# Kernel tuning notes

Hardware: AMD Instinct MI355X
Metric: run time of the kernel (lower is better)

## Reference

```python
import jax, jax.numpy as jnp
import numpy as np

VOCAB, E, S, H, L = 32000, 1024, 2048, 16, 2
HS = E // H  # head_size = 64
EPS = 1e-5


def setup_inputs() -> dict:
    key = jax.random.key(0)
    ks = jax.random.split(key, 12)
    sc = 0.02
    inp = {
        "seq": jax.random.randint(ks[0], (S,), 0, VOCAB, dtype=jnp.int64)
        if jax.config.jax_enable_x64 else jax.random.randint(ks[0], (S,), 0, VOCAB, dtype=jnp.int32),
        "tok_emb": jax.random.normal(ks[1], (VOCAB, E), jnp.float32) * sc,
        "pos_emb": jax.random.normal(ks[2], (S, E), jnp.float32) * sc,
        "Wq": jax.random.normal(ks[3], (L, H, E, HS), jnp.float32) * sc,
        "Wk": jax.random.normal(ks[4], (L, H, E, HS), jnp.float32) * sc,
        "Wv": jax.random.normal(ks[5], (L, H, E, HS), jnp.float32) * sc,
        "Wr": jax.random.normal(ks[6], (L, E, E), jnp.float32) * sc,
        "br": jnp.zeros((L, E), jnp.float32),
        "W1": jax.random.normal(ks[7], (L, E, 4 * E), jnp.float32) * sc,
        "b1": jnp.zeros((L, 4 * E), jnp.float32),
        "W2": jax.random.normal(ks[8], (L, 4 * E, E), jnp.float32) * sc,
        "b2": jnp.zeros((L, E), jnp.float32),
        "ln_g": jnp.ones((L, E), jnp.float32),
        "ln_b": jnp.zeros((L, E), jnp.float32),
    }
    return inp


def _layer_norm(x, g, b):
    mu = jnp.mean(x, axis=-1, keepdims=True)
    var = jnp.mean(jnp.square(x - mu), axis=-1, keepdims=True)
    return (x - mu) * jax.lax.rsqrt(var + EPS) * g + b


def reference(seq, tok_emb, pos_emb, Wq, Wk, Wv, Wr, br, W1, b1, W2, b2, ln_g, ln_b):
    # embeddings: [S, E]
    x = tok_emb[seq] + pos_emb
    att_maps = []
    for l in range(L):
        # NOTE: the torch Block reuses the SAME LayerNorm instance twice per block.
        x = _layer_norm(x, ln_g[l], ln_b[l])
        # per-head projections: [H, S, HS]
        q = jnp.einsum('se,hed->hsd', x, Wq[l])
        k = jnp.einsum('se,hed->hsd', x, Wk[l])
        v = jnp.einsum('se,hed->hsd', x, Wv[l])
        # unmasked (encoder) attention, full [H, S, S] scores
        atts = jax.nn.softmax(jnp.einsum('hsd,htd->hst', q, k) / np.sqrt(HS), axis=-1)
        av = jnp.einsum('hst,htd->hsd', atts, v)  # [H, S, HS]
        cat = jnp.transpose(av, (1, 0, 2)).reshape(S, H * HS)  # concat heads -> [S, E]
        x = x + cat @ Wr[l] + br[l]
        x = _layer_norm(x, ln_g[l], ln_b[l])
        x = x + jax.nn.relu(x @ W1[l] + b1[l]) @ W2[l] + b2[l]
        att_maps.append(atts)
    return x, jnp.stack(att_maps)  # ([S,E], [L,H,S,S])
```

## Files before the change

kernel.cpp:

```cpp
#include <hip/hip_runtime.h>
#include <hip/hip_bf16.h>


constexpr int S_ = 2048;
constexpr int E_ = 1024;
constexpr int H_ = 16;
constexpr int HS_ = 64;
constexpr int L_ = 2;
constexpr int FF_ = 4096;

typedef __bf16 bf16;
typedef __bf16 bf16x8 __attribute__((ext_vector_type(8)));
typedef __bf16 bf16x4 __attribute__((ext_vector_type(4)));
typedef float f32x4 __attribute__((ext_vector_type(4)));

__device__ __forceinline__ void gld16(const void* g, const void* l) {
  __builtin_amdgcn_global_load_lds(
      (const __attribute__((address_space(1))) unsigned int*)g,
      (__attribute__((address_space(3))) unsigned int*)l, 16, 0, 0);
}

__global__ __launch_bounds__(256) void embed_ln_k(const int* __restrict__ seq,
                                                  const float* __restrict__ tok,
                                                  const float* __restrict__ pos,
                                                  const float* __restrict__ gw,
                                                  const float* __restrict__ bw,
                                                  float* __restrict__ x,
                                                  bf16* __restrict__ xb) {
  __shared__ float red[8];
  const int row = blockIdx.x, tid = threadIdx.x;
  const int t = seq[row];
  float4 v = ((const float4*)(tok + (long)t * E_))[tid];
  float4 p = ((const float4*)(pos + (long)row * E_))[tid];
  v.x += p.x; v.y += p.y; v.z += p.z; v.w += p.w;
  float s = v.x + v.y + v.z + v.w;
  float ss = v.x * v.x + v.y * v.y + v.z * v.z + v.w * v.w;
  for (int off = 32; off; off >>= 1) {
    s += __shfl_down(s, off);
    ss += __shfl_down(ss, off);
  }
  if ((tid & 63) == 0) { red[(tid >> 6) * 2] = s; red[(tid >> 6) * 2 + 1] = ss; }
  __syncthreads();
  if (tid == 0) {
    float S0 = 0, SS = 0;
    for (int i = 0; i < 4; ++i) { S0 += red[i * 2]; SS += red[i * 2 + 1]; }
    red[0] = S0; red[1] = SS;
  }
  __syncthreads();
  const float mu = red[0] * (1.f / E_);
  const float var = red[1] * (1.f / E_) - mu * mu;
  const float rs = rsqrtf(var + 1e-5f);
  float4 gv = ((const float4*)gw)[tid], bv = ((const float4*)bw)[tid];
  float4 o;
  o.x = (v.x - mu) * rs * gv.x + bv.x;
  o.y = (v.y - mu) * rs * gv.y + bv.y;
  o.z = (v.z - mu) * rs * gv.z + bv.z;
  o.w = (v.w - mu) * rs * gv.w + bv.w;
  ((float4*)(x + (long)row * E_))[tid] = o;
  bf16x4 ob;
  ob[0] = (__bf16)o.x; ob[1] = (__bf16)o.y; ob[2] = (__bf16)o.z; ob[3] = (__bf16)o.w;
  ((bf16x4*)(xb + (long)row * E_))[tid] = ob;
}

__global__ __launch_bounds__(256) void layernorm_k(float* __restrict__ x,
                                                   const float* __restrict__ gw,
                                                   const float* __restrict__ bw,
                                                   bf16* __restrict__ xb) {
  __shared__ float red[8];
  const int row = blockIdx.x, tid = threadIdx.x;
  float4 v = ((const float4*)(x + (long)row * E_))[tid];
  float s = v.x + v.y + v.z + v.w;
  float ss = v.x * v.x + v.y * v.y + v.z * v.z + v.w * v.w;
  for (int off = 32; off; off >>= 1) {
    s += __shfl_down(s, off);
    ss += __shfl_down(ss, off);
  }
  if ((tid & 63) == 0) { red[(tid >> 6) * 2] = s; red[(tid >> 6) * 2 + 1] = ss; }
  __syncthreads();
  if (tid == 0) {
    float S0 = 0, SS = 0;
    for (int i = 0; i < 4; ++i) { S0 += red[i * 2]; SS += red[i * 2 + 1]; }
    red[0] = S0; red[1] = SS;
  }
  __syncthreads();
  const float mu = red[0] * (1.f / E_);
  const float var = red[1] * (1.f / E_) - mu * mu;
  const float rs = rsqrtf(var + 1e-5f);
  float4 gv = ((const float4*)gw)[tid], bv = ((const float4*)bw)[tid];
  float4 o;
  o.x = (v.x - mu) * rs * gv.x + bv.x;
  o.y = (v.y - mu) * rs * gv.y + bv.y;
  o.z = (v.z - mu) * rs * gv.z + bv.z;
  o.w = (v.w - mu) * rs * gv.w + bv.w;
  ((float4*)(x + (long)row * E_))[tid] = o;
  bf16x4 ob;
  ob[0] = (__bf16)o.x; ob[1] = (__bf16)o.y; ob[2] = (__bf16)o.z; ob[3] = (__bf16)o.w;
  ((bf16x4*)(xb + (long)row * E_))[tid] = ob;
}

__global__ __launch_bounds__(256) void repack_k(const float* __restrict__ wq,
                                                const float* __restrict__ wk,
                                                const float* __restrict__ wv,
                                                const float* __restrict__ wr,
                                                const float* __restrict__ w1,
                                                const float* __restrict__ w2,
                                                bf16* __restrict__ qkvT,
                                                bf16* __restrict__ wrT,
                                                bf16* __restrict__ w1T,
                                                bf16* __restrict__ w2T) {
  __shared__ float t[32][33];
  const int tx = threadIdx.x, ty = threadIdx.y;
  const int bid = blockIdx.x;
  const float* src;
  bf16* dst;
  long ld_in, ld_out, r0, c0;
  if (bid < 3072) {
    const int j = bid >> 10;
    const int z = (bid & 1023) >> 6;
    const int rem = bid & 63;
    r0 = (rem >> 1) * 32;
    c0 = (rem & 1) * 32;
    const float* w = j == 0 ? wq : (j == 1 ? wk : wv);
    src = w + (long)z * E_ * HS_;
    dst = qkvT + (long)j * E_ * E_ + (long)z * HS_ * E_;
    ld_in = HS_; ld_out = E_;
  } else if (bid < 4096) {
    const int idx = bid - 3072;
    r0 = (idx >> 5) * 32; c0 = (idx & 31) * 32;
    src = wr; dst = wrT; ld_in = E_; ld_out = E_;
  } else if (bid < 8192) {
    const int idx = bid - 4096;
    r0 = (idx >> 7) * 32; c0 = (idx & 127) * 32;
    src = w1; dst = w1T; ld_in = FF_; ld_out = E_;
  } else {
    const int idx = bid - 8192;
    r0 = (idx >> 5) * 32; c0 = (idx & 31) * 32;
    src = w2; dst = w2T; ld_in = E_; ld_out = FF_;
  }
#pragma unroll
  for (int i = 0; i < 4; ++i)
    t[ty + 8 * i][tx] = src[(r0 + ty + 8 * i) * ld_in + c0 + tx];
  __syncthreads();
#pragma unroll
  for (int i = 0; i < 4; ++i)
    dst[(c0 + ty + 8 * i) * ld_out + r0 + tx] = (__bf16)t[tx][ty + 8 * i];
}

__global__ __launch_bounds__(256) void trans_b2b(const bf16* __restrict__ in,
                                                 bf16* __restrict__ out,
                                                 long ld_in, long ld_out) {
  __shared__ bf16 t[32][33];
  const int tx = threadIdx.x, ty = threadIdx.y;
  const long r0 = (long)blockIdx.x * 32, c0 = (long)blockIdx.y * 32;
#pragma unroll
  for (int i = 0; i < 4; ++i)
    t[ty + 8 * i][tx] = in[(r0 + ty + 8 * i) * ld_in + c0 + tx];
  __syncthreads();
#pragma unroll
  for (int i = 0; i < 4; ++i)
    out[(c0 + ty + 8 * i) * ld_out + r0 + tx] = t[tx][ty + 8 * i];
}

template <int WM, int WN>
__global__ __launch_bounds__(WM * WN * 64) void gemm_lds(
    const bf16* __restrict__ A, const bf16* __restrict__ B,
    long lda, long ldb, int K, int mtiles, float scale,
    const float* __restrict__ bias, const float* __restrict__ resid, int relu,
    float* __restrict__ Cf, long ldc, bf16* __restrict__ Cb, long ldcb) {
  constexpr int BM = WM * 64, BN = WN * 64, NW = WM * WN;
  constexpr int ABYTES = BM * 64;
  constexpr int BUFB = ABYTES + BN * 64;
  constexpr int NCH = BUFB / 1024;
  constexpr int CPT = NCH / NW;
  static_assert(CPT == 4 || CPT == 6, "unexpected CPT");
  __shared__ char smem[3 * BUFB];

  const int tid = threadIdx.x, wid = tid >> 6, lane = tid & 63;
  const int cpx = gridDim.x >> 3;
  const int bid = blockIdx.x;
  const int wg = (bid & 7) * cpx + (bid >> 3);
  const long m0 = (long)(wg % mtiles) * BM;
  const long n0 = (long)(wg / mtiles) * BN;

  const char* gsrc[CPT];
  int ldsbase[CPT];
#pragma unroll
  for (int i = 0; i < CPT; ++i) {
    const int c = wid + i * NW;
    const int s = c * 1024 + lane * 16;
    const bf16* base;
    int kb;
    if (s < ABYTES) {
      const int row = s >> 6;
      kb = (s ^ ((row & 3) << 4)) & 63;
      base = A + (m0 + row) * lda;
    } else {
      const int s2 = s - ABYTES;
      const int row = s2 >> 6;
      kb = (s2 ^ ((row & 3) << 4)) & 63;
      base = B + (n0 + row) * ldb;
    }
    gsrc[i] = (const char*)base + kb;
    ldsbase[i] = c * 1024;
  }

  const int fr = lane & 15, fg = lane >> 4;
  const int wm = wid % WM, wn = wid / WM;
  int aoff[4], boff[4];
#pragma unroll
  for (int t = 0; t < 4; ++t) {
    const int m = wm * 64 + t * 16 + fr;
    aoff[t] = m * 64 + ((16 * fg) ^ ((m & 3) << 4));
    const int n = wn * 64 + t * 16 + fr;
    boff[t] = ABYTES + n * 64 + ((16 * fg) ^ ((n & 3) << 4));
  }

  f32x4 acc[4][4];
#pragma unroll
  for (int i = 0; i < 4; ++i)
#pragma unroll
    for (int j = 0; j < 4; ++j) acc[i][j] = (f32x4){0.f, 0.f, 0.f, 0.f};

  const int nt = K >> 5;

  auto stage = [&](int tile, int buf) {
    const long koff = (long)tile * 64;
#pragma unroll
    for (int i = 0; i < CPT; ++i)
      gld16(gsrc[i] + koff, smem + buf * BUFB + ldsbase[i]);
  };

  stage(0, 0);
  stage(1, 1);

  int cur = 0;
  for (int t = 0; t < nt; ++t) {
    if (t < nt - 1) {
      if constexpr (CPT == 4) asm volatile("s_waitcnt vmcnt(4)" ::: "memory");
      else asm volatile("s_waitcnt vmcnt(6)" ::: "memory");
    } else {
      asm volatile("s_waitcnt vmcnt(0)" ::: "memory");
    }
    __builtin_amdgcn_s_barrier();
    if (t + 2 < nt) {
      int sb = cur + 2; if (sb >= 3) sb -= 3;
      stage(t + 2, sb);
    }
    const char* sbuf = smem + cur * BUFB;
    bf16x8 a[4], b[4];
#pragma unroll
    for (int i = 0; i < 4; ++i) a[i] = *(const bf16x8*)(sbuf + aoff[i]);
#pragma unroll
    for (int i = 0; i < 4; ++i) b[i] = *(const bf16x8*)(sbuf + boff[i]);
#pragma unroll
    for (int i = 0; i < 4; ++i)
#pragma unroll
      for (int j = 0; j < 4; ++j)
        acc[i][j] = __builtin_amdgcn_mfma_f32_16x16x32_bf16(a[i], b[j], acc[i][j], 0, 0, 0);
    cur = cur + 1; if (cur >= 3) cur -= 3;
  }

#pragma unroll
  for (int tm = 0; tm < 4; ++tm) {
#pragma unroll
    for (int tn = 0; tn < 4; ++tn) {
      const long col = n0 + wn * 64 + tn * 16 + fr;
#pragma unroll
      for (int i = 0; i < 4; ++i) {
        const long row = m0 + wm * 64 + tm * 16 + fg * 4 + i;
        float v = acc[tm][tn][i] * scale;
        if (bias) v += bias[col];
        if (relu) v = v > 0.f ? v : 0.f;
        if (resid) v += resid[row * ldc + col];
        if (Cf) Cf[row * ldc + col] = v;
        if (Cb) Cb[row * ldcb + col] = (__bf16)v;
      }
    }
  }
}

__global__ __launch_bounds__(256, 2) void attn_fused(
    const bf16* __restrict__ qkv,
    const bf16* __restrict__ vt,
    float* __restrict__ att,
    bf16* __restrict__ avb) {
  constexpr int QB = 64, KB = 128;
  constexpr int NKT = S_ / KB;
  constexpr float C2 = 0.1803368801111244f;
  __shared__ char plds[QB * 256];

  const int tid = threadIdx.x, lane = tid & 63, w = tid >> 6;
  const int fr = lane & 15, fg = lane >> 4;
  const int bid = blockIdx.x;
  const int wg = (bid & 7) * 64 + (bid >> 3);
  const int h = wg >> 5;
  const long q0 = (long)(wg & 31) * QB;
  const int q = w * 16 + fr;
  const int swz = (q & 15) << 4;

  bf16x8 qf[2];
#pragma unroll
  for (int k0 = 0; k0 < 2; ++k0)
    qf[k0] = *(const bf16x8*)(qkv + (q0 + q) * (3 * E_) + h * HS_ + k0 * 32 + fg * 8);

  float l_ = 0.f;

  for (int kt = 0; kt < NKT; ++kt) {
    const long t0 = (long)kt * KB;
    bf16x8 kf[8][2];
#pragma unroll
    for (int mt = 0; mt < 8; ++mt)
#pragma unroll
      for (int k0 = 0; k0 < 2; ++k0)
        kf[mt][k0] = *(const bf16x8*)(qkv + (t0 + mt * 16 + fr) * (3 * E_) +
                                      E_ + h * HS_ + k0 * 32 + fg * 8);
    f32x4 acc[8];
#pragma unroll
    for (int mt = 0; mt < 8; ++mt) acc[mt] = (f32x4){0.f, 0.f, 0.f, 0.f};
#pragma unroll
    for (int k0 = 0; k0 < 2; ++k0)
#pragma unroll
      for (int mt = 0; mt < 8; ++mt)
        acc[mt] = __builtin_amdgcn_mfma_f32_16x16x32_bf16(kf[mt][k0], qf[k0], acc[mt], 0, 0, 0);
    float sum = 0.f;
#pragma unroll
    for (int mt = 0; mt < 8; ++mt)
#pragma unroll
      for (int i = 0; i < 4; ++i) sum += __builtin_amdgcn_exp2f(acc[mt][i] * C2);
    l_ += sum;
  }
  l_ += __shfl_xor(l_, 16);
  l_ += __shfl_xor(l_, 32);
  const float invl = 1.f / l_;

  f32x4 ao[4];
#pragma unroll
  for (int d = 0; d < 4; ++d) ao[d] = (f32x4){0.f, 0.f, 0.f, 0.f};

  for (int kt = 0; kt < NKT; ++kt) {
    const long t0 = (long)kt * KB;
    bf16x8 kf[8][2];
#pragma unroll
    for (int mt = 0; mt < 8; ++mt)
#pragma unroll
      for (int k0 = 0; k0 < 2; ++k0)
        kf[mt][k0] = *(const bf16x8*)(qkv + (t0 + mt * 16 + fr) * (3 * E_) +
                                      E_ + h * HS_ + k0 * 32 + fg * 8);
    f32x4 acc[8];
#pragma unroll
    for (int mt = 0; mt < 8; ++mt) acc[mt] = (f32x4){0.f, 0.f, 0.f, 0.f};
#pragma unroll
    for (int k0 = 0; k0 < 2; ++k0)
#pragma unroll
      for (int mt = 0; mt < 8; ++mt)
        acc[mt] = __builtin_amdgcn_mfma_f32_16x16x32_bf16(kf[mt][k0], qf[k0], acc[mt], 0, 0, 0);

    float* arow = att + ((long)h * S_ + q0 + q) * S_ + t0;
#pragma unroll
    for (int mt = 0; mt < 8; ++mt) {
      f32x4 pv;
#pragma unroll
      for (int i = 0; i < 4; ++i)
        pv[i] = __builtin_amdgcn_exp2f(acc[mt][i] * C2) * invl;
      __builtin_nontemporal_store(pv, (f32x4*)(arow + mt * 16 + fg * 4));
      bf16x4 pb;
      pb[0] = (__bf16)pv[0]; pb[1] = (__bf16)pv[1];
      pb[2] = (__bf16)pv[2]; pb[3] = (__bf16)pv[3];
      const int tb = (mt * 16 + fg * 4) * 2;
      *(bf16x4*)(plds + q * 256 + ((tb & ~15) ^ swz) + (tb & 15)) = pb;
    }
    __syncthreads();

#pragma unroll
    for (int k0 = 0; k0 < 4; ++k0) {
      const bf16x8 bq = *(const bf16x8*)(plds + q * 256 + ((k0 * 64 + fg * 16) ^ swz));
#pragma unroll
      for (int dmt = 0; dmt < 4; ++dmt) {
        bf16x8 av = *(const bf16x8*)(vt + (long)(h * HS_ + dmt * 16 + fr) * S_ +
                                     t0 + k0 * 32 + fg * 8);
        ao[dmt] = __builtin_amdgcn_mfma_f32_16x16x32_bf16(av, bq, ao[dmt], 0, 0, 0);
      }
    }
    __syncthreads();
  }

#pragma unroll
  for (int dmt = 0; dmt < 4; ++dmt) {
    bf16x4 o;
    o[0] = (__bf16)ao[dmt][0]; o[1] = (__bf16)ao[dmt][1];
    o[2] = (__bf16)ao[dmt][2]; o[3] = (__bf16)ao[dmt][3];
    *(bf16x4*)(avb + (q0 + q) * E_ + h * HS_ + dmt * 16 + fg * 4) = o;
  }
}

extern "C" void kernel_launch(void* const* d_in, const int* in_sizes, int n_in,
                              void* d_out, int out_size, void* d_ws, size_t ws_size,
                              hipStream_t stream) {
  const int* seq = (const int*)d_in[0];
  const float* tok_emb = (const float*)d_in[1];
  const float* pos_emb = (const float*)d_in[2];
  const float* Wq = (const float*)d_in[3];
  const float* Wk = (const float*)d_in[4];
  const float* Wv = (const float*)d_in[5];
  const float* Wr = (const float*)d_in[6];
  const float* br = (const float*)d_in[7];
  const float* W1 = (const float*)d_in[8];
  const float* b1 = (const float*)d_in[9];
  const float* W2 = (const float*)d_in[10];
  const float* b2 = (const float*)d_in[11];
  const float* ln_g = (const float*)d_in[12];
  const float* ln_b = (const float*)d_in[13];

  float* outx = (float*)d_out;
  float* att_all = outx + (long)S_ * E_;

  char* w = (char*)d_ws;
  auto alloc = [&](size_t bytes) {
    char* p = w;
    w += (bytes + 255) & ~(size_t)255;
    return p;
  };
  float* x = (float*)alloc((size_t)S_ * E_ * 4);
  bf16* xb = (bf16*)alloc((size_t)S_ * E_ * 2);
  bf16* qkvb = (bf16*)alloc((size_t)S_ * 3 * E_ * 2);
  bf16* vt = (bf16*)alloc((size_t)E_ * S_ * 2);
  bf16* avb = (bf16*)alloc((size_t)S_ * E_ * 2);
  bf16* hb = (bf16*)alloc((size_t)S_ * FF_ * 2);
  bf16* wqkvT = (bf16*)alloc((size_t)3 * E_ * E_ * 2);
  bf16* wrT = (bf16*)alloc((size_t)E_ * E_ * 2);
  bf16* w1T = (bf16*)alloc((size_t)E_ * FF_ * 2);
  bf16* w2T = (bf16*)alloc((size_t)E_ * FF_ * 2);
  (void)ws_size; (void)in_sizes; (void)n_in; (void)out_size;

  embed_ln_k<<<S_, 256, 0, stream>>>(seq, tok_emb, pos_emb, ln_g, ln_b, x, xb);

  for (int l = 0; l < L_; ++l) {
    repack_k<<<12288, dim3(32, 8, 1), 0, stream>>>(
        Wq + (long)l * H_ * E_ * HS_, Wk + (long)l * H_ * E_ * HS_,
        Wv + (long)l * H_ * E_ * HS_, Wr + (long)l * E_ * E_,
        W1 + (long)l * E_ * FF_, W2 + (long)l * FF_ * E_,
        wqkvT, wrT, w1T, w2T);

    if (l > 0)
      layernorm_k<<<S_, 256, 0, stream>>>(x, ln_g + (long)l * E_, ln_b + (long)l * E_, xb);

    gemm_lds<2, 2><<<dim3(16 * 24), 256, 0, stream>>>(
        xb, wqkvT, E_, E_, E_, 16, 1.f, nullptr, nullptr, 0,
        nullptr, 0, qkvb, 3 * E_);

    trans_b2b<<<dim3(S_ / 32, E_ / 32, 1), dim3(32, 8, 1), 0, stream>>>(
        qkvb + 2 * E_, vt, 3 * E_, S_);

    float* att_l = att_all + (long)l * H_ * S_ * S_;
    attn_fused<<<512, 256, 0, stream>>>(qkvb, vt, att_l, avb);

    gemm_lds<2, 1><<<dim3(16 * 16), 128, 0, stream>>>(
        avb, wrT, E_, E_, E_, 16, 1.f, br + (long)l * E_, x, 0,
        x, E_, nullptr, 0);

    layernorm_k<<<S_, 256, 0, stream>>>(x, ln_g + (long)l * E_, ln_b + (long)l * E_, xb);

    gemm_lds<2, 2><<<dim3(16 * 32), 256, 0, stream>>>(
        xb, w1T, E_, E_, E_, 16, 1.f, b1 + (long)l * FF_, nullptr, 1,
        nullptr, 0, hb, FF_);

    float* xdst = (l == L_ - 1) ? outx : x;
    gemm_lds<2, 1><<<dim3(16 * 16), 128, 0, stream>>>(
        hb, w2T, FF_, FF_, FF_, 16, 1.f, b2 + (long)l * E_, x, 0,
        xdst, E_, nullptr, 0);
  }
}
```

Measured before the change: 764.7 us.

## Fuse V transpose into QKV GEMM, use 32x32 MFMA, trim attention barriers

The GEMM kernel now uses 32x32x16 bf16 MFMA tiles with 16-wide accumulators instead of 16x16x32 tiles, which reduces LDS fragment loads per MFMA. The QKV GEMM epilogue writes the V columns straight into the transposed vt buffer, removing the separate trans_b2b kernel and its round trip through memory. In attention, the softmax normalisation is folded into the exp2 argument as a log-sum offset, and both per-iteration __syncthreads around the P staging buffer are dropped. Dropping those barriers is only safe if each wave reads back only the LDS rows it wrote itself.

```diff
diff --git a/kernel.cpp b/kernel.cpp
--- a/kernel.cpp
+++ b/kernel.cpp
@@ -13,6 +13,7 @@
 typedef __bf16 bf16x8 __attribute__((ext_vector_type(8)));
 typedef __bf16 bf16x4 __attribute__((ext_vector_type(4)));
 typedef float f32x4 __attribute__((ext_vector_type(4)));
+typedef float f32x16 __attribute__((ext_vector_type(16)));
 
 __device__ __forceinline__ void gld16(const void* g, const void* l) {
   __builtin_amdgcn_global_load_lds(
@@ -146,27 +147,13 @@
     dst[(c0 + ty + 8 * i) * ld_out + r0 + tx] = (__bf16)t[tx][ty + 8 * i];
 }
 
-__global__ __launch_bounds__(256) void trans_b2b(const bf16* __restrict__ in,
-                                                 bf16* __restrict__ out,
-                                                 long ld_in, long ld_out) {
-  __shared__ bf16 t[32][33];
-  const int tx = threadIdx.x, ty = threadIdx.y;
-  const long r0 = (long)blockIdx.x * 32, c0 = (long)blockIdx.y * 32;
-#pragma unroll
-  for (int i = 0; i < 4; ++i)
-    t[ty + 8 * i][tx] = in[(r0 + ty + 8 * i) * ld_in + c0 + tx];
-  __syncthreads();
-#pragma unroll
-  for (int i = 0; i < 4; ++i)
-    out[(c0 + ty + 8 * i) * ld_out + r0 + tx] = t[tx][ty + 8 * i];
-}
-
 template <int WM, int WN>
 __global__ __launch_bounds__(WM * WN * 64) void gemm_lds(
     const bf16* __restrict__ A, const bf16* __restrict__ B,
     long lda, long ldb, int K, int mtiles, float scale,
     const float* __restrict__ bias, const float* __restrict__ resid, int relu,
-    float* __restrict__ Cf, long ldc, bf16* __restrict__ Cb, long ldcb) {
+    float* __restrict__ Cf, long ldc, bf16* __restrict__ Cb, long ldcb,
+    bf16* __restrict__ Vt, long vthresh) {
   constexpr int BM = WM * 64, BN = WN * 64, NW = WM * WN;
   constexpr int ABYTES = BM * 64;
   constexpr int BUFB = ABYTES + BN * 64;
@@ -204,22 +191,26 @@
     ldsbase[i] = c * 1024;
   }
 
-  const int fr = lane & 15, fg = lane >> 4;
+  const int r5 = lane & 31, g2 = lane >> 5;
   const int wm = wid % WM, wn = wid / WM;
-  int aoff[4], boff[4];
-#pragma unroll
-  for (int t = 0; t < 4; ++t) {
-    const int m = wm * 64 + t * 16 + fr;
-    aoff[t] = m * 64 + ((16 * fg) ^ ((m & 3) << 4));
-    const int n = wn * 64 + t * 16 + fr;
-    boff[t] = ABYTES + n * 64 + ((16 * fg) ^ ((n & 3) << 4));
-  }
-
-  f32x4 acc[4][4];
-#pragma unroll
-  for (int i = 0; i < 4; ++i)
-#pragma unroll
-    for (int j = 0; j < 4; ++j) acc[i][j] = (f32x4){0.f, 0.f, 0.f, 0.f};
+  int aoff[2][2], boff[2][2];
+#pragma unroll
+  for (int tm = 0; tm < 2; ++tm)
+#pragma unroll
+    for (int kh = 0; kh < 2; ++kh) {
+      const int m = wm * 64 + tm * 32 + r5;
+      aoff[tm][kh] = m * 64 + ((kh * 32 + g2 * 16) ^ ((m & 3) << 4));
+      const int n = wn * 64 + tm * 32 + r5;
+      boff[tm][kh] = ABYTES + n * 64 + ((kh * 32 + g2 * 16) ^ ((n & 3) << 4));
+    }
+
+  f32x16 acc[2][2];
+#pragma unroll
+  for (int i = 0; i < 2; ++i)
+#pragma unroll
+    for (int j = 0; j < 2; ++j)
+#pragma unroll
+      for (int r = 0; r < 16; ++r) acc[i][j][r] = 0.f;
 
   const int nt = K >> 5;
 
@@ -247,33 +238,50 @@
       stage(t + 2, sb);
     }
     const char* sbuf = smem + cur * BUFB;
-    bf16x8 a[4], b[4];
-#pragma unroll
-    for (int i = 0; i < 4; ++i) a[i] = *(const bf16x8*)(sbuf + aoff[i]);
-#pragma unroll
-    for (int i = 0; i < 4; ++i) b[i] = *(const bf16x8*)(sbuf + boff[i]);
-#pragma unroll
-    for (int i = 0; i < 4; ++i)
-#pragma unroll
-      for (int j = 0; j < 4; ++j)
-        acc[i][j] = __builtin_amdgcn_mfma_f32_16x16x32_bf16(a[i], b[j], acc[i][j], 0, 0, 0);
+    bf16x8 a[2][2], b[2][2];
+#pragma unroll
+    for (int i = 0; i < 2; ++i)
+#pragma unroll
+      for (int kh = 0; kh < 2; ++kh) {
+        a[i][kh] = *(const bf16x8*)(sbuf + aoff[i][kh]);
+        b[i][kh] = *(const bf16x8*)(sbuf + boff[i][kh]);
+      }
+#pragma unroll
+    for (int kh = 0; kh < 2; ++kh)
+#pragma unroll
+      for (int i = 0; i < 2; ++i)
+#pragma unroll
+        for (int j = 0; j < 2; ++j)
+          acc[i][j] = __builtin_amdgcn_mfma_f32_32x32x16_bf16(a[i][kh], b[j][kh], acc[i][j], 0, 0, 0);
     cur = cur + 1; if (cur >= 3) cur -= 3;
   }
 
 #pragma unroll
-  for (int tm = 0; tm < 4; ++tm) {
-#pragma unroll
-    for (int tn = 0; tn < 4; ++tn) {
-      const long col = n0 + wn * 64 + tn * 16 + fr;
-#pragma unroll
-      for (int i = 0; i < 4; ++i) {
-        const long row = m0 + wm * 64 + tm * 16 + fg * 4 + i;
-        float v = acc[tm][tn][i] * scale;
-        if (bias) v += bias[col];
-        if (relu) v = v > 0.f ? v : 0.f;
-        if (resid) v += resid[row * ldc + col];
-        if (Cf) Cf[row * ldc + col] = v;
-        if (Cb) Cb[row * ldcb + col] = (__bf16)v;
+  for (int tm = 0; tm < 2; ++tm) {
+#pragma unroll
+    for (int tn = 0; tn < 2; ++tn) {
+      const long col = n0 + wn * 64 + tn * 32 + r5;
+      const long rowb = m0 + wm * 64 + tm * 32 + 4 * g2;
+      if (Vt && col >= vthresh) {
+        bf16* vdst = Vt + (col - vthresh) * (long)S_ + rowb;
+#pragma unroll
+        for (int g = 0; g < 4; ++g) {
+          bf16x4 o;
+#pragma unroll
+          for (int i = 0; i < 4; ++i) o[i] = (__bf16)(acc[tm][tn][g * 4 + i]);
+          *(bf16x4*)(vdst + g * 8) = o;
+        }
+      } else {
+#pragma unroll
+        for (int r = 0; r < 16; ++r) {
+          const long row = rowb + (r & 3) + 8 * (r >> 2);
+          float v = acc[tm][tn][r] * scale;
+          if (bias) v += bias[col];
+          if (relu) v = v > 0.f ? v : 0.f;
+          if (resid) v += resid[row * ldc + col];
+          if (Cf) Cf[row * ldc + col] = v;
+          if (Cb) Cb[row * ldcb + col] = (__bf16)v;
+        }
       }
     }
   }
@@ -331,6 +339,7 @@
   }
   l_ += __shfl_xor(l_, 16);
   l_ += __shfl_xor(l_, 32);
+  const float li = -__log2f(l_);
   const float invl = 1.f / l_;
 
   f32x4 ao[4];
@@ -361,7 +370,7 @@
       f32x4 pv;
 #pragma unroll
       for (int i = 0; i < 4; ++i)
-        pv[i] = __builtin_amdgcn_exp2f(acc[mt][i] * C2) * invl;
+        pv[i] = __builtin_amdgcn_exp2f(fmaf(acc[mt][i], C2, li));
       __builtin_nontemporal_store(pv, (f32x4*)(arow + mt * 16 + fg * 4));
       bf16x4 pb;
       pb[0] = (__bf16)pv[0]; pb[1] = (__bf16)pv[1];
@@ -369,7 +378,6 @@
       const int tb = (mt * 16 + fg * 4) * 2;
       *(bf16x4*)(plds + q * 256 + ((tb & ~15) ^ swz) + (tb & 15)) = pb;
     }
-    __syncthreads();
 
 #pragma unroll
     for (int k0 = 0; k0 < 4; ++k0) {
@@ -381,8 +389,8 @@
         ao[dmt] = __builtin_amdgcn_mfma_f32_16x16x32_bf16(av, bq, ao[dmt], 0, 0, 0);
       }
     }
-    __syncthreads();
-  }
+  }
+  (void)invl;
 
 #pragma unroll
   for (int dmt = 0; dmt < 4; ++dmt) {
@@ -446,27 +454,24 @@
 
     gemm_lds<2, 2><<<dim3(16 * 24), 256, 0, stream>>>(
         xb, wqkvT, E_, E_, E_, 16, 1.f, nullptr, nullptr, 0,
-        nullptr, 0, qkvb, 3 * E_);
-
-    trans_b2b<<<dim3(S_ / 32, E_ / 32, 1), dim3(32, 8, 1), 0, stream>>>(
-        qkvb + 2 * E_, vt, 3 * E_, S_);
+        nullptr, 0, qkvb, 3 * E_, vt, 2 * E_);
 
     float* att_l = att_all + (long)l * H_ * S_ * S_;
     attn_fused<<<512, 256, 0, stream>>>(qkvb, vt, att_l, avb);
 
     gemm_lds<2, 1><<<dim3(16 * 16), 128, 0, stream>>>(
         avb, wrT, E_, E_, E_, 16, 1.f, br + (long)l * E_, x, 0,
-        x, E_, nullptr, 0);
+        x, E_, nullptr, 0, nullptr, 0x7fffffff);
 
     layernorm_k<<<S_, 256, 0, stream>>>(x, ln_g + (long)l * E_, ln_b + (long)l * E_, xb);
 
     gemm_lds<2, 2><<<dim3(16 * 32), 256, 0, stream>>>(
         xb, w1T, E_, E_, E_, 16, 1.f, b1 + (long)l * FF_, nullptr, 1,
-        nullptr, 0, hb, FF_);
+        nullptr, 0, hb, FF_, nullptr, 0x7fffffff);
 
     float* xdst = (l == L_ - 1) ? outx : x;
     gemm_lds<2, 1><<<dim3(16 * 16), 128, 0, stream>>>(
         hb, w2T, FF_, FF_, FF_, 16, 1.f, b2 + (long)l * E_, x, 0,
-        xdst, E_, nullptr, 0);
-  }
-}
+        xdst, E_, nullptr, 0, nullptr, 0x7fffffff);
+  }
+}
```

New measurement: 815.0 us. +6.6%, slower.

## Add intra-block K-split GEMM for N=1024 projections and trim attention syncs

Applied to the files above, without the earlier changes.

Adds a gemm_ksplit kernel for the output projection and FFN down-projection. It uses 64x64 tiles, and each of the four waves covers a quarter of K with its own double-buffered LDS region, loaded by direct global-to-LDS transfers. The four partial sums are then reduced through LDS. This doubles the block count for these N=1024 GEMMs to raise occupancy and CU coverage. The attention kernel now folds the softmax normalization into the exp2 argument via a negative log2 of the row sum. It also drops both per-tile __syncthreads, since each wave only reads its own P rows in LDS. The trade-offs are an extra LDS reduction in the GEMM and a slight change in rounding for the normalization.

```diff
diff --git a/kernel.cpp b/kernel.cpp
--- a/kernel.cpp
+++ b/kernel.cpp
@@ -279,6 +279,109 @@
   }
 }
 
+__global__ __launch_bounds__(256, 2) void gemm_ksplit(
+    const bf16* __restrict__ A, const bf16* __restrict__ B,
+    long lda, long ldb, int K, int mtiles, float scale,
+    const float* __restrict__ bias, const float* __restrict__ resid, int relu,
+    float* __restrict__ Cf, long ldc, bf16* __restrict__ Cb, long ldcb) {
+  __shared__ char smem[4 * 16384];
+
+  const int tid = threadIdx.x, w = tid >> 6, lane = tid & 63;
+  const int cpx = gridDim.x >> 3;
+  const int bid = blockIdx.x;
+  const int wg = (bid & 7) * cpx + (bid >> 3);
+  const long m0 = (long)(wg % mtiles) * 64;
+  const long n0 = (long)(wg / mtiles) * 64;
+  const int Kq = K >> 2;
+  const long k0w = (long)w * Kq;
+
+  const char* gsrc[8];
+  int ldsoff[8];
+#pragma unroll
+  for (int i = 0; i < 8; ++i) {
+    const int s = (i & 3) * 1024 + lane * 16;
+    const int row = s >> 6;
+    const int kb = (s ^ ((row & 3) << 4)) & 63;
+    const bf16* base = (i < 4) ? (A + (m0 + row) * lda + k0w)
+                               : (B + (n0 + row) * ldb + k0w);
+    gsrc[i] = (const char*)base + kb;
+    ldsoff[i] = w * 16384 + i * 1024;
+  }
+
+  const int fr = lane & 15, fg = lane >> 4;
+  int aoff[4], boff[4];
+#pragma unroll
+  for (int t = 0; t < 4; ++t) {
+    const int m = t * 16 + fr;
+    aoff[t] = w * 16384 + m * 64 + ((16 * fg) ^ ((m & 3) << 4));
+    boff[t] = aoff[t] + 4096;
+  }
+
+  f32x4 acc[4][4];
+#pragma unroll
+  for (int i = 0; i < 4; ++i)
+#pragma unroll
+    for (int j = 0; j < 4; ++j) acc[i][j] = (f32x4){0.f, 0.f, 0.f, 0.f};
+
+  const int nt = Kq >> 5;
+
+  auto stage = [&](int tile, int buf) {
+    const long koff = (long)tile * 64;
+#pragma unroll
+    for (int i = 0; i < 8; ++i)
+      gld16(gsrc[i] + koff, smem + ldsoff[i] + buf * 8192);
+  };
+
+  stage(0, 0);
+  if (nt > 1) stage(1, 1);
+
+  for (int t = 0; t < nt; ++t) {
+    if (t + 1 < nt) asm volatile("s_waitcnt vmcnt(8)" ::: "memory");
+    else asm volatile("s_waitcnt vmcnt(0)" ::: "memory");
+    const int bsel = (t & 1) * 8192;
+    bf16x8 a[4], b[4];
+#pragma unroll
+    for (int i = 0; i < 4; ++i) a[i] = *(const bf16x8*)(smem + aoff[i] + bsel);
+#pragma unroll
+    for (int i = 0; i < 4; ++i) b[i] = *(const bf16x8*)(smem + boff[i] + bsel);
+#pragma unroll
+    for (int i = 0; i < 4; ++i)
+#pragma unroll
+      for (int j = 0; j < 4; ++j)
+        acc[i][j] = __builtin_amdgcn_mfma_f32_16x16x32_bf16(a[i], b[j], acc[i][j], 0, 0, 0);
+    if (t + 2 < nt) stage(t + 2, t & 1);
+  }
+
+  __syncthreads();
+#pragma unroll
+  for (int f = 0; f < 16; ++f)
+    *(f32x4*)(smem + w * 16384 + f * 1024 + lane * 16) = acc[f >> 2][f & 3];
+  __syncthreads();
+
+#pragma unroll
+  for (int tn = 0; tn < 4; ++tn) {
+    const int f = w * 4 + tn;
+    f32x4 v0 = *(const f32x4*)(smem + 0 * 16384 + f * 1024 + lane * 16);
+    f32x4 v1 = *(const f32x4*)(smem + 1 * 16384 + f * 1024 + lane * 16);
+    f32x4 v2 = *(const f32x4*)(smem + 2 * 16384 + f * 1024 + lane * 16);
+    f32x4 v3 = *(const f32x4*)(smem + 3 * 16384 + f * 1024 + lane * 16);
+    f32x4 sv;
+#pragma unroll
+    for (int i = 0; i < 4; ++i) sv[i] = v0[i] + v1[i] + v2[i] + v3[i];
+    const long col = n0 + tn * 16 + fr;
+#pragma unroll
+    for (int i = 0; i < 4; ++i) {
+      const long row = m0 + w * 16 + fg * 4 + i;
+      float v = sv[i] * scale;
+      if (bias) v += bias[col];
+      if (relu) v = v > 0.f ? v : 0.f;
+      if (resid) v += resid[row * ldc + col];
+      if (Cf) Cf[row * ldc + col] = v;
+      if (Cb) Cb[row * ldcb + col] = (__bf16)v;
+    }
+  }
+}
+
 __global__ __launch_bounds__(256, 2) void attn_fused(
     const bf16* __restrict__ qkv,
     const bf16* __restrict__ vt,
@@ -331,7 +434,7 @@
   }
   l_ += __shfl_xor(l_, 16);
   l_ += __shfl_xor(l_, 32);
-  const float invl = 1.f / l_;
+  const float li = -__log2f(l_);
 
   f32x4 ao[4];
 #pragma unroll
@@ -361,7 +464,7 @@
       f32x4 pv;
 #pragma unroll
       for (int i = 0; i < 4; ++i)
-        pv[i] = __builtin_amdgcn_exp2f(acc[mt][i] * C2) * invl;
+        pv[i] = __builtin_amdgcn_exp2f(fmaf(acc[mt][i], C2, li));
       __builtin_nontemporal_store(pv, (f32x4*)(arow + mt * 16 + fg * 4));
       bf16x4 pb;
       pb[0] = (__bf16)pv[0]; pb[1] = (__bf16)pv[1];
@@ -369,7 +472,6 @@
       const int tb = (mt * 16 + fg * 4) * 2;
       *(bf16x4*)(plds + q * 256 + ((tb & ~15) ^ swz) + (tb & 15)) = pb;
     }
-    __syncthreads();
 
 #pragma unroll
     for (int k0 = 0; k0 < 4; ++k0) {
@@ -381,7 +483,6 @@
         ao[dmt] = __builtin_amdgcn_mfma_f32_16x16x32_bf16(av, bq, ao[dmt], 0, 0, 0);
       }
     }
-    __syncthreads();
   }
 
 #pragma unroll
@@ -454,8 +555,8 @@
     float* att_l = att_all + (long)l * H_ * S_ * S_;
     attn_fused<<<512, 256, 0, stream>>>(qkvb, vt, att_l, avb);
 
-    gemm_lds<2, 1><<<dim3(16 * 16), 128, 0, stream>>>(
-        avb, wrT, E_, E_, E_, 16, 1.f, br + (long)l * E_, x, 0,
+    gemm_ksplit<<<32 * 16, 256, 0, stream>>>(
+        avb, wrT, E_, E_, E_, 32, 1.f, br + (long)l * E_, x, 0,
         x, E_, nullptr, 0);
 
     layernorm_k<<<S_, 256, 0, stream>>>(x, ln_g + (long)l * E_, ln_b + (long)l * E_, xb);
@@ -465,8 +566,8 @@
         nullptr, 0, hb, FF_);
 
     float* xdst = (l == L_ - 1) ? outx : x;
-    gemm_lds<2, 1><<<dim3(16 * 16), 128, 0, stream>>>(
-        hb, w2T, FF_, FF_, FF_, 16, 1.f, b2 + (long)l * E_, x, 0,
+    gemm_ksplit<<<32 * 16, 256, 0, stream>>>(
+        hb, w2T, FF_, FF_, FF_, 32, 1.f, b2 + (long)l * E_, x, 0,
         xdst, E_, nullptr, 0);
   }
 }
```

After: 699.6 us. -8.5%, faster.
